# Kernel tuning notes

Hardware: AMD Instinct MI355X
Metric: run time of the kernel (lower is better)

The kernel has to match this reference:

```python
import jax, jax.numpy as jnp
import numpy as np

GH, GW = 64, 64          # grid_size
NUM_OBJ = 16             # num_objects
FEAT = 256               # feature_dim
DECAY = 0.95             # decay_factor
B = 4                    # batch


def setup_inputs() -> dict:
    key = jax.random.key(0)
    ks = jax.random.split(key, 6)
    return {
        "grid_state": jax.random.normal(ks[0], (B, GH, GW, NUM_OBJ, FEAT), jnp.float32),
        "grid_confidence": jax.random.uniform(ks[1], (B, GH, GW, NUM_OBJ), jnp.float32),
        "grid_temporal": jax.random.uniform(ks[2], (B, GH, GW, NUM_OBJ), jnp.float32),
        "object_features": jax.random.normal(ks[3], (B, NUM_OBJ, FEAT), jnp.float32),
        "positions": jax.random.uniform(ks[4], (B, NUM_OBJ, 2), jnp.float32),  # normalized (x, y) in [0,1)
        "occlusion_factors": jax.random.uniform(ks[5], (B, NUM_OBJ), jnp.float32),
    }


def reference(grid_state, grid_confidence, grid_temporal,
              object_features, positions, occlusion_factors):
    """Vectorized SpatialMemoryGrid.update_grid.

    Indices (b, gh, gw, obj) are unique per (b, obj) because obj is a grid axis,
    so the original nested Python loop is an exact gather -> blend -> scatter-set.
    Returns grid_state, confidence, temporal packed along the last axis:
    [B, GH, GW, N, F+2].
    """
    Bsz, gh_dim, gw_dim, nobj, fdim = grid_state.shape
    cmax = max(gh_dim, gw_dim) - 1
    # position_to_grid: scale, clamp (as float, like torch), then truncate to int
    gw = jnp.clip(positions[..., 0] * (gw_dim - 1), 0, cmax).astype(jnp.int32)  # [B, N]
    gh = jnp.clip(positions[..., 1] * (gh_dim - 1), 0, cmax).astype(jnp.int32)  # [B, N]
    b = jnp.arange(Bsz)[:, None]      # [B, 1]
    o = jnp.arange(nobj)[None, :]     # [1, N]

    cur_feat = grid_state[b, gh, gw, o]        # [B, N, F] gather
    cur_conf = grid_confidence[b, gh, gw, o]   # [B, N]

    visible = occlusion_factors < 0.5          # [B, N]
    alpha = jnp.where(visible, 0.8, 0.3)[..., None]
    new_feat = alpha * object_features + (1.0 - alpha) * cur_feat
    new_conf = jnp.where(visible,
                         jnp.minimum(1.0, cur_conf * 0.9 + 0.5),
                         cur_conf * DECAY)
    temporal_inc = jnp.where(visible, 1.0, 0.5)

    state = grid_state.at[b, gh, gw, o].set(new_feat)
    conf = grid_confidence.at[b, gh, gw, o].set(new_conf) * DECAY  # global decay applied last
    temp = grid_temporal.at[b, gh, gw, o].add(temporal_inc)

    return jnp.concatenate([state, conf[..., None], temp[..., None]], axis=-1)
```

## Files before the change

### kernel.cpp

```cpp
#include <hip/hip_runtime.h>


#define GH 64
#define GW 64
#define NOBJ 16
#define FEAT 256
#define DECAYF 0.95f

__global__ __launch_bounds__(256) void smg_kernel(
    const float* __restrict__ grid_state,
    const float* __restrict__ grid_conf,
    const float* __restrict__ grid_temp,
    const float* __restrict__ obj_feat,
    const float* __restrict__ positions,
    const float* __restrict__ occl,
    float* __restrict__ out)
{
    const int cell = blockIdx.x * 2 + (threadIdx.x >> 7);
    const int t    = threadIdx.x & 127;

    const int o  = cell & (NOBJ - 1);
    const int gw = (cell >> 4) & (GW - 1);
    const int gh = (cell >> 10) & (GH - 1);
    const int b  = cell >> 16;
    const int bo = b * NOBJ + o;

    const float px = positions[bo * 2 + 0];
    const float py = positions[bo * 2 + 1];
    const int gwt = (int)fminf(fmaxf(px * (float)(GW - 1), 0.0f), 63.0f);
    const int ght = (int)fminf(fmaxf(py * (float)(GH - 1), 0.0f), 63.0f);
    const bool upd = (gw == gwt) && (gh == ght);

    const float2* __restrict__ sp = (const float2*)grid_state + (size_t)cell * (FEAT / 2);
    float*        __restrict__ ob = out + (size_t)cell * (FEAT + 2);
    float2*       __restrict__ op = (float2*)ob;

    float2 v = sp[t];

    if (upd) {
        const bool  vis   = occl[bo] < 0.5f;
        const float alpha = vis ? 0.8f : 0.3f;
        const float beta  = 1.0f - alpha;
        const float2 w = ((const float2*)obj_feat + (size_t)bo * (FEAT / 2))[t];
        v.x = alpha * w.x + beta * v.x;
        v.y = alpha * w.y + beta * v.y;
    }
    op[t] = v;

    if (t == 0) {
        float c  = grid_conf[cell];
        float tm = grid_temp[cell];
        if (upd) {
            const bool vis = occl[bo] < 0.5f;
            c  = vis ? fminf(1.0f, c * 0.9f + 0.5f) : c * DECAYF;
            tm += vis ? 1.0f : 0.5f;
        }
        float2 ct;
        ct.x = c * DECAYF;
        ct.y = tm;
        ((float2*)(ob + FEAT))[0] = ct;
    }
}

extern "C" void kernel_launch(void* const* d_in, const int* in_sizes, int n_in,
                              void* d_out, int out_size, void* d_ws, size_t ws_size,
                              hipStream_t stream) {
    const float* grid_state = (const float*)d_in[0];
    const float* grid_conf  = (const float*)d_in[1];
    const float* grid_temp  = (const float*)d_in[2];
    const float* obj_feat   = (const float*)d_in[3];
    const float* positions  = (const float*)d_in[4];
    const float* occl       = (const float*)d_in[5];
    float* out = (float*)d_out;

    const int B = in_sizes[5] / NOBJ;
    const int cells = B * GH * GW * NOBJ;
    const int blocks = cells / 2;

    smg_kernel<<<blocks, 256, 0, stream>>>(grid_state, grid_conf, grid_temp,
                                           obj_feat, positions, occl, out);
}
```

Measured before the change: 446.2 us.

## Split into a float4 packed copy kernel plus a sparse per-object fixup kernel

Replaces the per-cell kernel with two kernels. The first is a fully coalesced float4 copy that packs the state, decayed confidence and temporal values for pairs of cells into the 258-float output stride. The second is a small kernel that rewrites only the B*NOBJ updated cells with the blended features and updated confidence and temporal values. This removes the per-thread position and update checks and the float2 writes from the bulk copy, at the cost of a second launch, stream-ordered overwrites of already-written cells, and a mixed gather pattern for odd cells.

```diff
diff --git a/kernel.cpp b/kernel.cpp
--- a/kernel.cpp
+++ b/kernel.cpp
@@ -7,58 +7,88 @@
 #define FEAT 256
 #define DECAYF 0.95f
 
-__global__ __launch_bounds__(256) void smg_kernel(
-    const float* __restrict__ grid_state,
-    const float* __restrict__ grid_conf,
-    const float* __restrict__ grid_temp,
-    const float* __restrict__ obj_feat,
-    const float* __restrict__ positions,
-    const float* __restrict__ occl,
-    float* __restrict__ out)
+__global__ __launch_bounds__(256) void smg_pack(
+    const float4* __restrict__ state4,
+    const float2* __restrict__ state2,
+    const float*  __restrict__ conf,
+    const float*  __restrict__ temp,
+    float4*       __restrict__ out4,
+    int total4)
 {
-    const int cell = blockIdx.x * 2 + (threadIdx.x >> 7);
-    const int t    = threadIdx.x & 127;
+    const int tid = blockIdx.x * 256 + threadIdx.x;
+    if (tid >= total4) return;
+    const unsigned q = (unsigned)tid / 129u;
+    const unsigned j = (unsigned)tid - q * 129u;
+    const unsigned cellE = 2u * q;
+    const unsigned cellO = cellE + 1u;
 
-    const int o  = cell & (NOBJ - 1);
-    const int gw = (cell >> 4) & (GW - 1);
-    const int gh = (cell >> 10) & (GH - 1);
-    const int b  = cell >> 16;
-    const int bo = b * NOBJ + o;
+    float4 v;
+    if (j < 64u) {
+        v = state4[(size_t)cellE * 64u + j];
+    } else if (j == 64u) {
+        const float2 s = state2[(size_t)cellO * 128u];
+        v.x = conf[cellE] * DECAYF;
+        v.y = temp[cellE];
+        v.z = s.x;
+        v.w = s.y;
+    } else if (j < 128u) {
+        const unsigned k = j - 65u;
+        const size_t base = (size_t)cellO * 128u;
+        const float2 a = state2[base + 2u * k + 1u];
+        const float2 b = state2[base + 2u * k + 2u];
+        v.x = a.x; v.y = a.y; v.z = b.x; v.w = b.y;
+    } else {
+        const float2 s = state2[(size_t)cellO * 128u + 127u];
+        v.x = s.x;
+        v.y = s.y;
+        v.z = conf[cellO] * DECAYF;
+        v.w = temp[cellO];
+    }
+    out4[tid] = v;
+}
 
-    const float px = positions[bo * 2 + 0];
-    const float py = positions[bo * 2 + 1];
+__global__ __launch_bounds__(64) void smg_fixup(
+    const float*  __restrict__ state,
+    const float*  __restrict__ conf,
+    const float*  __restrict__ temp,
+    const float*  __restrict__ objf,
+    const float*  __restrict__ pos,
+    const float*  __restrict__ occl,
+    float*        __restrict__ out)
+{
+    const int bo = blockIdx.x;
+    const int b  = bo >> 4;
+    const int o  = bo & (NOBJ - 1);
+
+    const float px = pos[bo * 2 + 0];
+    const float py = pos[bo * 2 + 1];
     const int gwt = (int)fminf(fmaxf(px * (float)(GW - 1), 0.0f), 63.0f);
     const int ght = (int)fminf(fmaxf(py * (float)(GH - 1), 0.0f), 63.0f);
-    const bool upd = (gw == gwt) && (gh == ght);
+    const int cell = ((b * GH + ght) * GW + gwt) * NOBJ + o;
 
-    const float2* __restrict__ sp = (const float2*)grid_state + (size_t)cell * (FEAT / 2);
-    float*        __restrict__ ob = out + (size_t)cell * (FEAT + 2);
-    float2*       __restrict__ op = (float2*)ob;
+    const bool  vis   = occl[bo] < 0.5f;
+    const float alpha = vis ? 0.8f : 0.3f;
+    const float beta  = 1.0f - alpha;
 
-    float2 v = sp[t];
+    const int i = threadIdx.x;
+    const float4 w = ((const float4*)objf)[bo * 64 + i];
+    const float4 s = ((const float4*)state)[(size_t)cell * 64 + i];
+    float4 r;
+    r.x = alpha * w.x + beta * s.x;
+    r.y = alpha * w.y + beta * s.y;
+    r.z = alpha * w.z + beta * s.z;
+    r.w = alpha * w.w + beta * s.w;
 
-    if (upd) {
-        const bool  vis   = occl[bo] < 0.5f;
-        const float alpha = vis ? 0.8f : 0.3f;
-        const float beta  = 1.0f - alpha;
-        const float2 w = ((const float2*)obj_feat + (size_t)bo * (FEAT / 2))[t];
-        v.x = alpha * w.x + beta * v.x;
-        v.y = alpha * w.y + beta * v.y;
-    }
-    op[t] = v;
+    float* ob = out + (size_t)cell * (FEAT + 2) + 4 * i;
+    ((float2*)ob)[0] = make_float2(r.x, r.y);
+    ((float2*)ob)[1] = make_float2(r.z, r.w);
 
-    if (t == 0) {
-        float c  = grid_conf[cell];
-        float tm = grid_temp[cell];
-        if (upd) {
-            const bool vis = occl[bo] < 0.5f;
-            c  = vis ? fminf(1.0f, c * 0.9f + 0.5f) : c * DECAYF;
-            tm += vis ? 1.0f : 0.5f;
-        }
-        float2 ct;
-        ct.x = c * DECAYF;
-        ct.y = tm;
-        ((float2*)(ob + FEAT))[0] = ct;
+    if (i == 0) {
+        float c = conf[cell];
+        c = vis ? fminf(1.0f, c * 0.9f + 0.5f) : c * DECAYF;
+        const float t = temp[cell] + (vis ? 1.0f : 0.5f);
+        ((float2*)(out + (size_t)cell * (FEAT + 2) + FEAT))[0] =
+            make_float2(c * DECAYF, t);
     }
 }
 
@@ -73,10 +103,15 @@
     const float* occl       = (const float*)d_in[5];
     float* out = (float*)d_out;
 
-    const int B = in_sizes[5] / NOBJ;
-    const int cells = B * GH * GW * NOBJ;
-    const int blocks = cells / 2;
+    const int B      = in_sizes[5] / NOBJ;
+    const int cells  = B * GH * GW * NOBJ;
+    const int total4 = (cells / 2) * 129;
+    const int blocks = (total4 + 255) / 256;
 
-    smg_kernel<<<blocks, 256, 0, stream>>>(grid_state, grid_conf, grid_temp,
-                                           obj_feat, positions, occl, out);
+    smg_pack<<<blocks, 256, 0, stream>>>(
+        (const float4*)grid_state, (const float2*)grid_state,
+        grid_conf, grid_temp, (float4*)out, total4);
+
+    smg_fixup<<<B * NOBJ, 64, 0, stream>>>(
+        grid_state, grid_conf, grid_temp, obj_feat, positions, occl, out);
 }
```

Result: no change. 450.0 us (+0.9%).
